# Kernel tuning notes

Hardware: AMD Instinct MI355X
Metric: run time of the kernel (lower is better)

## Reference

```python
import jax, jax.numpy as jnp
import numpy as np


def setup_inputs() -> dict:
    key = jax.random.key(0)
    k1, k2, k3, k4 = jax.random.split(key, 4)
    B, C_ORIG, H, W = 64, 448, 56, 56
    C = 100
    P = H * W
    feats = jax.random.normal(k1, (B, C_ORIG, H, W), dtype=jnp.float32)
    mean = jax.random.normal(k2, (P, C), dtype=jnp.float32)
    icov = jax.random.normal(k3, (P, C, C), dtype=jnp.float32)
    sel_idx = jnp.sort(jax.random.randint(k4, (C,), 0, C_ORIG, dtype=jnp.int64))
    return {"feats": feats, "mean": mean, "icov": icov, "sel_idx": sel_idx,
            "image_size": 224}


def reference(feats, mean, icov, sel_idx, image_size):
    # feats: [B, C_orig, H, W]; select the PaDiM random channel subset -> [B, C, H, W]
    f = feats[:, sel_idx]
    B, C, H, W = f.shape
    # [B, H*W, C] patch-major layout as in the torch code
    f = jnp.transpose(f, (0, 2, 3, 1)).reshape(B, H * W, C)
    # Per-patch Mahalanobis distance, fully batched over all H*W patches
    # (replaces the Python loop of H*W small einsums in the original).
    diff = f - mean[None]                                   # [B, P, C]
    dist = jnp.einsum('bpi,pij,bpj->bp', diff, icov, diff)  # [B, P]
    score_map = dist.reshape(B, H, W)
    # Bilinear upsample to input resolution (align_corners=False ~ half-pixel)
    score_map = jax.image.resize(score_map, (B, image_size, image_size),
                                 method='bilinear')
    return score_map
```

## Files before the change

kernel.cpp:

```cpp
#include <hip/hip_runtime.h>
#include <hip/hip_bf16.h>

#define B_N     64
#define C_ORIG  448
#define C_SEL   100
#define CPD     112
#define HW      3136
#define IMG     224

typedef short bf16x8 __attribute__((ext_vector_type(8)));
typedef float f32x4  __attribute__((ext_vector_type(4)));

static __device__ __forceinline__ unsigned pkbf(float x, float y) {
    union { __hip_bfloat162 h; unsigned u; } c;
    c.h = __float22bfloat162_rn(float2{x, y});
    return c.u;
}
static __device__ __forceinline__ float bf2f(unsigned short h) {
    return __uint_as_float(((unsigned int)h) << 16);
}

__global__ __launch_bounds__(256) void kA0_meanT(const float* __restrict__ mean,
                                                 float* __restrict__ meanT)
{
    __shared__ float mt[64 * 100];
    const int tid = threadIdx.x;
    const int p0  = blockIdx.x * 64;
    const float4* src = reinterpret_cast<const float4*>(mean + (size_t)p0 * C_SEL);
#pragma unroll
    for (int q = 0; q < 7; ++q) {
        int idx4 = tid + q * 256;
        if (idx4 < 1600) {
            float4 v = src[idx4];
            *reinterpret_cast<float4*>(&mt[idx4 * 4]) = v;
        }
    }
    __syncthreads();
#pragma unroll
    for (int q = 0; q < 7; ++q) {
        int u = tid + q * 256;
        if (u < 1600) {
            int c = u >> 4, s = u & 15;
            float4 v;
            v.x = mt[(s * 4 + 0) * 100 + c];
            v.y = mt[(s * 4 + 1) * 100 + c];
            v.z = mt[(s * 4 + 2) * 100 + c];
            v.w = mt[(s * 4 + 3) * 100 + c];
            *reinterpret_cast<float4*>(meanT + (size_t)c * HW + p0 + s * 4) = v;
        }
    }
}

__global__ __launch_bounds__(256) void kA_gather(const float* __restrict__ feats,
                                                 const float* __restrict__ meanT,
                                                 const int* __restrict__ sel,
                                                 unsigned short* __restrict__ D)
{
    __shared__ unsigned short Dt[64 * 128];
    char* DtB = reinterpret_cast<char*>(Dt);
    const int tid = threadIdx.x;
    const int p0  = blockIdx.x * 64;
    const int b   = blockIdx.y;

    if (tid < 192) {
        int pr = tid / 3, un = 25 + tid % 3;
        *reinterpret_cast<uint2*>(DtB + pr * 256 + ((8 * un) ^ ((pr & 31) << 3)))
            = make_uint2(0u, 0u);
    }

    const int w    = tid >> 6;
    const int lane = tid & 63;
    const float* fb = feats + (size_t)b * (C_ORIG * HW) + p0 + lane;
    const float* mb = meanT + p0 + lane;
    const unsigned swz = (unsigned)(lane & 31) << 3;
    char* rowB = DtB + lane * 256;

    auto quad = [&](int c0) {
        int ch0 = sel[c0], ch1 = sel[c0 + 1], ch2 = sel[c0 + 2], ch3 = sel[c0 + 3];
        float v0 = fb[(size_t)ch0 * HW] - mb[(size_t)(c0 + 0) * HW];
        float v1 = fb[(size_t)ch1 * HW] - mb[(size_t)(c0 + 1) * HW];
        float v2 = fb[(size_t)ch2 * HW] - mb[(size_t)(c0 + 2) * HW];
        float v3 = fb[(size_t)ch3 * HW] - mb[(size_t)(c0 + 3) * HW];
        uint2 pk = make_uint2(pkbf(v0, v1), pkbf(v2, v3));
        *reinterpret_cast<uint2*>(rowB + (((unsigned)(2 * c0)) ^ swz)) = pk;
    };

    if (w < 3) {
#pragma unroll
        for (int q = 0; q < 6; ++q) quad(w * 24 + q * 4);
    } else {
#pragma unroll
        for (int q = 0; q < 7; ++q) quad(72 + q * 4);
    }
    __syncthreads();

    unsigned short* Dp = D + ((size_t)p0 * B_N + b) * CPD;
#pragma unroll
    for (int q = 0; q < 4; ++q) {
        int unit = tid + q * 256;
        if (unit < 896) {
            int pr = unit / 14;
            int s  = unit % 14;
            unsigned off = ((unsigned)(16 * s)) ^ ((((unsigned)pr & 31u) << 3) & 0xF0u);
            uint4 v = *reinterpret_cast<const uint4*>(DtB + pr * 256 + off);
            uint4 r = (pr & 1) ? make_uint4(v.z, v.w, v.x, v.y) : v;
            *reinterpret_cast<uint4*>(reinterpret_cast<char*>(Dp)
                + (size_t)pr * (B_N * CPD * 2) + s * 16) = r;
        }
    }
}

__global__ __launch_bounds__(256, 6) void kB_maha(const float* __restrict__ icov,
                                                  const unsigned short* __restrict__ D,
                                                  float* __restrict__ dist)
{
    __shared__ unsigned short Mb[100 * 128];
    char* MbB = reinterpret_cast<char*>(Mb);
    const int tid  = threadIdx.x;
    const int p    = blockIdx.x;
    const int w    = tid >> 6;
    const int lane = tid & 63;
    const int lrow = lane & 15;
    const int g    = lane >> 4;
    const int bcol = w * 16 + lrow;
    const unsigned short* Drow = D + ((size_t)p * B_N + bcol) * CPD;

    bf16x8 bfr[4];
#pragma unroll
    for (int ks = 0; ks < 4; ++ks)
        bfr[ks] = *reinterpret_cast<const bf16x8*>(Drow + ks * 32 + g * 8);

#pragma unroll
    for (int q = 0; q < 3; ++q) {
        int z = tid + q * 256;
        if (z < 700) {
            int i = z / 7, un = 25 + z % 7;
            *reinterpret_cast<uint2*>(MbB + i * 256 + ((8 * un) ^ ((i & 7) << 4)))
                = make_uint2(0u, 0u);
        }
    }
    const float4* src = reinterpret_cast<const float4*>(icov + (size_t)p * (C_SEL * C_SEL));
#pragma unroll
    for (int q = 0; q < 10; ++q) {
        int idx4 = tid + q * 256;
        if (idx4 < 2500) {
            float4 v = src[idx4];
            int i = idx4 / 25, un = idx4 % 25;
            uint2 pk = make_uint2(pkbf(v.x, v.y), pkbf(v.z, v.w));
            *reinterpret_cast<uint2*>(MbB + i * 256 + ((8 * un) ^ ((i & 7) << 4))) = pk;
        }
    }
    __syncthreads();

    ushort4 dvec[7];
#pragma unroll
    for (int it = 0; it < 7; ++it)
        dvec[it] = *reinterpret_cast<const ushort4*>(Drow + it * 16 + g * 4);

    f32x4 acc[7];
#pragma unroll
    for (int it = 0; it < 7; ++it) acc[it] = (f32x4){0.f, 0.f, 0.f, 0.f};

#pragma unroll
    for (int ks = 0; ks < 4; ++ks) {
#pragma unroll
        for (int it = 0; it < 7; ++it) {
            bf16x8 afrag = {};
            if (it < 6 || lrow < 4) {
                int i = it * 16 + lrow;
                afrag = *reinterpret_cast<const bf16x8*>(
                    MbB + i * 256 + ((ks * 64 + g * 16) ^ ((i & 7) << 4)));
            }
            acc[it] = __builtin_amdgcn_mfma_f32_16x16x32_bf16(afrag, bfr[ks], acc[it], 0, 0, 0);
        }
    }

    float partial = 0.f;
#pragma unroll
    for (int it = 0; it < 7; ++it) {
#pragma unroll
        for (int r = 0; r < 4; ++r) {
            int i = it * 16 + g * 4 + r;
            if (i < C_SEL) {
                unsigned short dh = (r == 0) ? dvec[it].x : (r == 1) ? dvec[it].y
                                   : (r == 2) ? dvec[it].z : dvec[it].w;
                partial += acc[it][r] * bf2f(dh);
            }
        }
    }
    partial += __shfl_xor(partial, 16);
    partial += __shfl_xor(partial, 32);
    if (g == 0) dist[p * B_N + bcol] = partial;
}

__global__ __launch_bounds__(256) void kC_resize(const float* __restrict__ dist,
                                                 float* __restrict__ out)
{
    __shared__ float L[2 * 56 * 34];
    const int tid  = threadIdx.x;
    const int y    = blockIdx.x;
    const int half = blockIdx.y;

    float sy = y * 0.25f - 0.375f;
    float fy0 = floorf(sy);
    float fy = sy - fy0;
    int y0 = max((int)fy0, 0);
    int y1 = min((int)fy0 + 1, 55);
    int rsrc[2] = {y0, y1};

#pragma unroll
    for (int r = 0; r < 2; ++r) {
        const float4* s4 = reinterpret_cast<const float4*>(dist + (size_t)rsrc[r] * 56 * B_N);
#pragma unroll
        for (int j = 0; j < 2; ++j) {
            int idx = tid + j * 256;
            if (idx < 448) {
                int m = idx >> 3;
                int k = idx & 7;
                float4 v = s4[m * 16 + half * 8 + k];
                float* d = &L[r * 56 * 34 + m * 34 + k * 4];
                d[0] = v.x; d[1] = v.y; d[2] = v.z; d[3] = v.w;
            }
        }
    }
    __syncthreads();

#pragma unroll
    for (int j = 0; j < 7; ++j) {
        int unit = tid + j * 256;
        int b = unit / 56;
        int m = unit % 56;
        int xm1 = max(m - 1, 0);
        int xp1 = min(m + 1, 55);

        const float* L0 = &L[0 * 56 * 34];
        const float* L1 = &L[1 * 56 * 34];
        float a0 = L0[xm1 * 34 + b], b0 = L0[m * 34 + b], c0 = L0[xp1 * 34 + b];
        float a1 = L1[xm1 * 34 + b], b1 = L1[m * 34 + b], c1 = L1[xp1 * 34 + b];

        float A  = a0 + fy * (a1 - a0);
        float Bv = b0 + fy * (b1 - b0);
        float Cv = c0 + fy * (c1 - c0);

        float4 o;
        o.x = A  + 0.625f * (Bv - A);
        o.y = A  + 0.875f * (Bv - A);
        o.z = Bv + 0.125f * (Cv - Bv);
        o.w = Bv + 0.375f * (Cv - Bv);
        *reinterpret_cast<float4*>(out + ((size_t)(half * 32 + b) * IMG + y) * IMG + 4 * m) = o;
    }
}

extern "C" void kernel_launch(void* const* d_in, const int* in_sizes, int n_in,
                              void* d_out, int out_size, void* d_ws, size_t ws_size,
                              hipStream_t stream)
{
    const float* feats = (const float*)d_in[0];
    const float* mean  = (const float*)d_in[1];
    const float* icov  = (const float*)d_in[2];
    const int*   sel   = (const int*)d_in[3];
    float* out = (float*)d_out;

    char* ws = (char*)d_ws;
    unsigned short* Dws = (unsigned short*)ws;
    size_t off = (size_t)HW * B_N * CPD * 2;
    float* distws = (float*)(ws + off);
    off += (size_t)HW * B_N * 4;
    float* meanT = (float*)(ws + off);

    kA0_meanT<<<49, 256, 0, stream>>>(mean, meanT);
    dim3 gA(49, B_N);
    kA_gather<<<gA, 256, 0, stream>>>(feats, meanT, sel, Dws);
    kB_maha<<<HW, 256, 0, stream>>>(icov, Dws, distws);
    dim3 gC(IMG, 2);
    kC_resize<<<gC, 256, 0, stream>>>(distws, out);
}
```

Measured before the change: 77.35 us.

## Stream icov to LDS via global_load_lds and convert to bf16 at fragment load

The Mahalanobis kernel now copies each patch's fp32 inverse covariance directly into shared memory with asynchronous global-to-LDS loads, then converts to bf16 while building MFMA fragments. This removes the register round trip and the packing pass the old staging path needed. The D intermediate is also shrunk from 112 to 104 channels of padding, which cuts gather store traffic and the matching read traffic. In exchange, LDS per block doubles to 40KB of fp32, occupancy is lowered to 4 blocks, the conversion now repeats inside the MFMA loop, and unswizzled fp32 reads may hit bank conflicts.

```diff
diff --git a/kernel.cpp b/kernel.cpp
--- a/kernel.cpp
+++ b/kernel.cpp
@@ -4,12 +4,13 @@
 #define B_N     64
 #define C_ORIG  448
 #define C_SEL   100
-#define CPD     112
+#define CPD     104
 #define HW      3136
 #define IMG     224
 
 typedef short bf16x8 __attribute__((ext_vector_type(8)));
 typedef float f32x4  __attribute__((ext_vector_type(4)));
+typedef unsigned int u32x4 __attribute__((ext_vector_type(4)));
 
 static __device__ __forceinline__ unsigned pkbf(float x, float y) {
     union { __hip_bfloat162 h; unsigned u; } c;
@@ -18,6 +19,11 @@
 }
 static __device__ __forceinline__ float bf2f(unsigned short h) {
     return __uint_as_float(((unsigned int)h) << 16);
+}
+static __device__ __forceinline__ void gld16(const void* g, void* l) {
+    __builtin_amdgcn_global_load_lds(
+        (const __attribute__((address_space(1))) unsigned int*)g,
+        (__attribute__((address_space(3))) unsigned int*)l, 16, 0, 0);
 }
 
 __global__ __launch_bounds__(256) void kA0_meanT(const float* __restrict__ mean,
@@ -62,9 +68,9 @@
     const int p0  = blockIdx.x * 64;
     const int b   = blockIdx.y;
 
-    if (tid < 192) {
-        int pr = tid / 3, un = 25 + tid % 3;
-        *reinterpret_cast<uint2*>(DtB + pr * 256 + ((8 * un) ^ ((pr & 31) << 3)))
+    if (tid < 64) {
+        int pr = tid;
+        *reinterpret_cast<uint2*>(DtB + pr * 256 + (200 ^ ((pr & 31) << 3)))
             = make_uint2(0u, 0u);
     }
 
@@ -94,28 +100,26 @@
     }
     __syncthreads();
 
-    unsigned short* Dp = D + ((size_t)p0 * B_N + b) * CPD;
+    char* DpB = reinterpret_cast<char*>(D) + ((size_t)p0 * B_N + b) * (CPD * 2);
 #pragma unroll
     for (int q = 0; q < 4; ++q) {
         int unit = tid + q * 256;
-        if (unit < 896) {
-            int pr = unit / 14;
-            int s  = unit % 14;
+        if (unit < 832) {
+            int pr = unit / 13;
+            int s  = unit % 13;
             unsigned off = ((unsigned)(16 * s)) ^ ((((unsigned)pr & 31u) << 3) & 0xF0u);
-            uint4 v = *reinterpret_cast<const uint4*>(DtB + pr * 256 + off);
-            uint4 r = (pr & 1) ? make_uint4(v.z, v.w, v.x, v.y) : v;
-            *reinterpret_cast<uint4*>(reinterpret_cast<char*>(Dp)
-                + (size_t)pr * (B_N * CPD * 2) + s * 16) = r;
-        }
-    }
-}
-
-__global__ __launch_bounds__(256, 6) void kB_maha(const float* __restrict__ icov,
+            u32x4 v = *reinterpret_cast<const u32x4*>(DtB + pr * 256 + off);
+            u32x4 r = (pr & 1) ? __builtin_shufflevector(v, v, 2, 3, 0, 1) : v;
+            *reinterpret_cast<u32x4*>(DpB + (size_t)pr * (B_N * CPD * 2) + s * 16) = r;
+        }
+    }
+}
+
+__global__ __launch_bounds__(256, 4) void kB_maha(const float* __restrict__ icov,
                                                   const unsigned short* __restrict__ D,
                                                   float* __restrict__ dist)
 {
-    __shared__ unsigned short Mb[100 * 128];
-    char* MbB = reinterpret_cast<char*>(Mb);
+    __shared__ float Mf[10000];
     const int tid  = threadIdx.x;
     const int p    = blockIdx.x;
     const int w    = tid >> 6;
@@ -125,31 +129,25 @@
     const int bcol = w * 16 + lrow;
     const unsigned short* Drow = D + ((size_t)p * B_N + bcol) * CPD;
 
+    {
+        const char* srcB = reinterpret_cast<const char*>(icov + (size_t)p * (C_SEL * C_SEL));
+        char* ldsB = reinterpret_cast<char*>(Mf);
+#pragma unroll
+        for (int q = 0; q < 10; ++q) {
+            int chunk = w * 10 + q;
+            if (chunk < 39) {
+                gld16(srcB + chunk * 1024 + lane * 16, ldsB + chunk * 1024);
+            } else if (lane < 4) {
+                gld16(srcB + 39 * 1024 + lane * 16, ldsB + 39 * 1024);
+            }
+        }
+    }
+
     bf16x8 bfr[4];
 #pragma unroll
     for (int ks = 0; ks < 4; ++ks)
         bfr[ks] = *reinterpret_cast<const bf16x8*>(Drow + ks * 32 + g * 8);
 
-#pragma unroll
-    for (int q = 0; q < 3; ++q) {
-        int z = tid + q * 256;
-        if (z < 700) {
-            int i = z / 7, un = 25 + z % 7;
-            *reinterpret_cast<uint2*>(MbB + i * 256 + ((8 * un) ^ ((i & 7) << 4)))
-                = make_uint2(0u, 0u);
-        }
-    }
-    const float4* src = reinterpret_cast<const float4*>(icov + (size_t)p * (C_SEL * C_SEL));
-#pragma unroll
-    for (int q = 0; q < 10; ++q) {
-        int idx4 = tid + q * 256;
-        if (idx4 < 2500) {
-            float4 v = src[idx4];
-            int i = idx4 / 25, un = idx4 % 25;
-            uint2 pk = make_uint2(pkbf(v.x, v.y), pkbf(v.z, v.w));
-            *reinterpret_cast<uint2*>(MbB + i * 256 + ((8 * un) ^ ((i & 7) << 4))) = pk;
-        }
-    }
     __syncthreads();
 
     ushort4 dvec[7];
@@ -165,13 +163,22 @@
     for (int ks = 0; ks < 4; ++ks) {
 #pragma unroll
         for (int it = 0; it < 7; ++it) {
-            bf16x8 afrag = {};
+            u32x4 u = {0u, 0u, 0u, 0u};
             if (it < 6 || lrow < 4) {
                 int i = it * 16 + lrow;
-                afrag = *reinterpret_cast<const bf16x8*>(
-                    MbB + i * 256 + ((ks * 64 + g * 16) ^ ((i & 7) << 4)));
-            }
-            acc[it] = __builtin_amdgcn_mfma_f32_16x16x32_bf16(afrag, bfr[ks], acc[it], 0, 0, 0);
+                const float* rp = &Mf[i * 100 + ks * 32 + g * 8];
+                if (ks < 3) {
+                    f32x4 a = *reinterpret_cast<const f32x4*>(rp);
+                    f32x4 bv = *reinterpret_cast<const f32x4*>(rp + 4);
+                    u[0] = pkbf(a[0], a[1]);  u[1] = pkbf(a[2], a[3]);
+                    u[2] = pkbf(bv[0], bv[1]); u[3] = pkbf(bv[2], bv[3]);
+                } else if (g == 0) {
+                    f32x4 a = *reinterpret_cast<const f32x4*>(rp);
+                    u[0] = pkbf(a[0], a[1]);  u[1] = pkbf(a[2], a[3]);
+                }
+            }
+            acc[it] = __builtin_amdgcn_mfma_f32_16x16x32_bf16(
+                __builtin_bit_cast(bf16x8, u), bfr[ks], acc[it], 0, 0, 0);
         }
     }
 
```

Result: faster. 72.31 us, median of 2 (-6.5%).
